# Kernel optimization log

Hardware: AMD Instinct MI355X
Metric: run time of the kernel (lower is better)

## Reference

```python
import jax, jax.numpy as jnp
import numpy as np

H = 8  # n_heads

def setup_inputs() -> dict:
    key = jax.random.key(0)
    k1, k2, k3, k4, k5 = jax.random.split(key, 5)
    B, N, D = 4, 2048, 512
    x = jax.random.normal(k1, (B, N, D), dtype=jnp.float32)
    mask_flat = jax.random.randint(k2, (B, N), 0, 2).astype(bool)
    s = 1.0 / np.sqrt(D)
    Wq = jax.random.normal(k3, (D, D), dtype=jnp.float32) * s
    Wkv = jax.random.normal(k4, (D, 2 * D), dtype=jnp.float32) * s
    Wo = jax.random.normal(k5, (D, D), dtype=jnp.float32) * s
    return {"x": x, "mask_flat": mask_flat, "Wq": Wq, "Wkv": Wkv, "Wo": Wo}

def reference(x, mask_flat, Wq, Wkv, Wo):
    B, N, D = x.shape
    d = D // H
    scale = d ** -0.5
    kv = x @ Wkv                                   # (B,N,2D)
    k, v = jnp.split(kv, 2, axis=-1)
    q = x @ Wq                                     # (B,N,D)
    # (B,H,N,d)
    q = q.reshape(B, N, H, d).transpose(0, 2, 1, 3)
    k = k.reshape(B, N, H, d).transpose(0, 2, 1, 3)
    v = v.reshape(B, N, H, d).transpose(0, 2, 1, 3)
    attn = jax.nn.softmax(jnp.einsum('bhmd,bhnd->bhmn', q, k) * scale, axis=-1)
    res = jnp.einsum('bhmn,bhnd->bhmd', attn, v)   # (B,H,N,d)
    out = res.transpose(0, 2, 1, 3).reshape(B, N, D) @ Wo
    # non-masked query positions produce zero output (residual elsewhere keeps them)
    return jnp.where(mask_flat[..., None], out, 0.0)
```

## Files before the change

kernel.cpp:

```cpp
#include <hip/hip_runtime.h>

typedef __bf16 bf16x8 __attribute__((ext_vector_type(8)));
typedef float f32x4 __attribute__((ext_vector_type(4)));
typedef float f32x16 __attribute__((ext_vector_type(16)));
typedef unsigned short u16x8 __attribute__((ext_vector_type(8)));
typedef unsigned short u16x4 __attribute__((ext_vector_type(4)));
typedef unsigned int u32x4 __attribute__((ext_vector_type(4)));
typedef int i32x2 __attribute__((ext_vector_type(2)));

__device__ inline unsigned short f2bf(float f) {
    __bf16 h = (__bf16)f;
    return __builtin_bit_cast(unsigned short, h);
}

__device__ inline unsigned int pkbf(float lo, float hi) {
    return (unsigned int)f2bf(lo) | ((unsigned int)f2bf(hi) << 16);
}

__device__ inline float fexp2(float x) {
#if __has_builtin(__builtin_amdgcn_exp2f)
    return __builtin_amdgcn_exp2f(x);
#else
    return exp2f(x);
#endif
}

__device__ inline f32x4 mfma16(u16x8 a, u16x8 b, f32x4 c) {
    return __builtin_amdgcn_mfma_f32_16x16x32_bf16(
        __builtin_bit_cast(bf16x8, a), __builtin_bit_cast(bf16x8, b), c, 0, 0, 0);
}

__device__ inline f32x16 mfma32(u16x8 a, u16x8 b, f32x16 c) {
    return __builtin_amdgcn_mfma_f32_32x32x16_bf16(
        __builtin_bit_cast(bf16x8, a), __builtin_bit_cast(bf16x8, b), c, 0, 0, 0);
}

__device__ inline i32x2 permswap(unsigned int a, unsigned int b, int hi) {
#if __has_builtin(__builtin_amdgcn_permlane32_swap)
    (void)hi;
    return __builtin_amdgcn_permlane32_swap((int)a, (int)b, false, false);
#else
    int pa_ = __shfl_xor((int)a, 32);
    int pb_ = __shfl_xor((int)b, 32);
    i32x2 r;
    r[0] = hi ? pb_ : (int)a;
    r[1] = hi ? (int)b : pa_;
    return r;
#endif
}

__device__ inline void gld_lds16(const unsigned short* gsrc, unsigned short* ldst) {
    __builtin_amdgcn_global_load_lds(
        (const __attribute__((address_space(1))) unsigned int*)gsrc,
        (__attribute__((address_space(3))) unsigned int*)ldst, 16, 0, 0);
}

#define WAIT_VM(n)                                          \
    asm volatile("s_waitcnt vmcnt(" #n ")" ::: "memory");   \
    __builtin_amdgcn_sched_barrier(0)
#define WAIT_LGKM0                                          \
    asm volatile("s_waitcnt lgkmcnt(0)" ::: "memory");      \
    __builtin_amdgcn_sched_barrier(0)
#define BARRIER                                             \
    __builtin_amdgcn_s_barrier();                           \
    __builtin_amdgcn_sched_barrier(0)

__global__ __launch_bounds__(256) void cvt_f32_bf16(const float* __restrict__ in,
                                                    unsigned short* __restrict__ out, long n) {
    long i = ((long)blockIdx.x * blockDim.x + threadIdx.x) * 4;
    if (i >= n) return;
    float4 v = *(const float4*)(in + i);
    ushort4 r;
    r.x = f2bf(v.x); r.y = f2bf(v.y); r.z = f2bf(v.z); r.w = f2bf(v.w);
    *(ushort4*)(out + i) = r;
}

__global__ __launch_bounds__(256) void prep_weights(const float* __restrict__ Wq,
                                                    const float* __restrict__ Wkv,
                                                    const float* __restrict__ Wo,
                                                    unsigned short* __restrict__ WqkvT,
                                                    unsigned short* __restrict__ WoT,
                                                    float qscale) {
    __shared__ float tile[64][65];
    const int z = blockIdx.z;
    if (z != 1 && blockIdx.x >= 8) return;
    const float* W = (z == 0) ? Wq : (z == 1) ? Wkv : Wo;
    unsigned short* Wt = (z == 0) ? WqkvT : (z == 1) ? (WqkvT + 512L * 512) : WoT;
    const int N = (z == 1) ? 1024 : 512;
    const float scale = (z == 0) ? qscale : 1.0f;
    const int K = 512;
    const int n0 = blockIdx.x * 64, k0 = blockIdx.y * 64;
    const int c = threadIdx.x & 63;
    const int r4 = threadIdx.x >> 6;
#pragma unroll
    for (int i = 0; i < 16; i++) {
        int r = r4 * 16 + i;
        tile[r][c] = W[(long)(k0 + r) * N + n0 + c];
    }
    __syncthreads();
#pragma unroll
    for (int i = 0; i < 16; i++) {
        int rr = r4 * 16 + i;
        Wt[(long)(n0 + rr) * K + k0 + c] = f2bf(tile[c][rr] * scale);
    }
}

__global__ __launch_bounds__(256) void scan_mask(const int* __restrict__ mask,
                                                 int* __restrict__ idx, int* __restrict__ cnt) {
    const int b = blockIdx.x;
    const int tid = threadIdx.x;
    __shared__ int wsum[4];
    int m[8]; int pc = 0;
#pragma unroll
    for (int k = 0; k < 8; k++) { m[k] = mask[b * 2048 + tid * 8 + k]; pc += (m[k] != 0); }
    int s = pc;
    const int lane = tid & 63;
    for (int off = 1; off < 64; off <<= 1) {
        int v = __shfl_up(s, off);
        if (lane >= off) s += v;
    }
    if (lane == 63) wsum[tid >> 6] = s;
    __syncthreads();
    int wbase = 0;
    for (int w = 0; w < (tid >> 6); w++) wbase += wsum[w];
    int run = wbase + s - pc;
#pragma unroll
    for (int k = 0; k < 8; k++) if (m[k]) idx[b * 2048 + (run++)] = tid * 8 + k;
    if (tid == 255) cnt[b] = wbase + s;
}

__global__ __launch_bounds__(256) void gemm_qkv(const unsigned short* __restrict__ A,
                                                const unsigned short* __restrict__ Bt,
                                                unsigned short* __restrict__ qkb,
                                                unsigned short* __restrict__ vT) {
    const int K = 512;
    __shared__ unsigned short AsL[2][128 * 32];
    __shared__ unsigned short BsL[2][128 * 32];
    const int tid = threadIdx.x;
    const int lane = tid & 63;
    const int wid = tid >> 6;
    const int lg = lane >> 4, lr = lane & 15;
    const int wm = wid >> 1, wn = wid & 1;
    const long m0 = (long)blockIdx.y * 128, n0 = (long)blockIdx.x * 128;

    f32x4 acc[4][4] = {};

    const unsigned short* aS0 = A  + (m0 + (tid >> 2)) * K + (tid & 3) * 8;
    const unsigned short* aS1 = A  + (m0 + 64 + (tid >> 2)) * K + (tid & 3) * 8;
    const unsigned short* bS0 = Bt + (n0 + (tid >> 2)) * K + (tid & 3) * 8;
    const unsigned short* bS1 = Bt + (n0 + 64 + (tid >> 2)) * K + (tid & 3) * 8;

#define GSTAGE(bufi, k0v)                                    \
    {                                                        \
        gld_lds16(aS0 + (k0v), &AsL[bufi][wid * 512]);       \
        gld_lds16(aS1 + (k0v), &AsL[bufi][2048 + wid * 512]);\
        gld_lds16(bS0 + (k0v), &BsL[bufi][wid * 512]);       \
        gld_lds16(bS1 + (k0v), &BsL[bufi][2048 + wid * 512]);\
    }
#define GREAD(cur)                                                                    \
    {                                                                                 \
        _Pragma("unroll")                                                             \
        for (int i = 0; i < 4; i++) {                                                 \
            af[i]  = *(const u16x8*)&AsL[cur][(wm * 64 + i * 16 + lr) * 32 + lg * 8]; \
            bfr[i] = *(const u16x8*)&BsL[cur][(wn * 64 + i * 16 + lr) * 32 + lg * 8]; \
        }                                                                             \
    }
#define GMFMA                                                                  \
    {                                                                          \
        _Pragma("unroll")                                                      \
        for (int i = 0; i < 4; i++)                                            \
            _Pragma("unroll")                                                  \
            for (int j = 0; j < 4; j++)                                        \
                acc[i][j] = mfma16(af[i], bfr[j], acc[i][j]);                  \
    }

    const int nk = K >> 5;
    GSTAGE(0, 0);
    GSTAGE(1, 32);
    for (int t = 0; t < nk - 1; t++) {
        const int cur = t & 1;
        u16x8 af[4], bfr[4];
        WAIT_VM(4);
        BARRIER;
        GREAD(cur);
        WAIT_LGKM0;
        BARRIER;
        if (t < nk - 2) GSTAGE(cur, (t + 2) * 32);
        GMFMA;
    }
    {
        u16x8 af[4], bfr[4];
        WAIT_VM(0);
        BARRIER;
        GREAD((nk - 1) & 1);
        GMFMA;
    }
#undef GSTAGE
#undef GREAD
#undef GMFMA

    if (n0 < 1024) {
#pragma unroll
        for (int i = 0; i < 4; i++)
#pragma unroll
            for (int j = 0; j < 4; j++)
#pragma unroll
                for (int r = 0; r < 4; r++) {
                    long row = m0 + wm * 64 + i * 16 + lg * 4 + r;
                    long col = n0 + wn * 64 + j * 16 + lr;
                    qkb[row * 1024 + col] = f2bf(acc[i][j][r]);
                }
    } else {
#pragma unroll
        for (int i = 0; i < 4; i++)
#pragma unroll
            for (int j = 0; j < 4; j++) {
                long vd = n0 - 1024 + wn * 64 + j * 16 + lr;
                long tok0 = m0 + wm * 64 + i * 16 + lg * 4;
                u16x4 st;
#pragma unroll
                for (int r = 0; r < 4; r++) st[r] = f2bf(acc[i][j][r]);
                *(u16x4*)&vT[vd * 8192 + tok0] = st;
            }
    }
}

template<int WRITE_BF16, int MASKED>
__global__ __launch_bounds__(256) void gemm_bt(const unsigned short* __restrict__ A,
                                               const unsigned short* __restrict__ Bt,
                                               void* __restrict__ Cv,
                                               int M, int N, int K,
                                               const int* __restrict__ mask) {
    __shared__ unsigned short AsL[2][128 * 32];
    __shared__ unsigned short BsL[2][128 * 32];
    const int tid = threadIdx.x;
    const int lane = tid & 63;
    const int wid = tid >> 6;
    const int lg = lane >> 4, lr = lane & 15;
    const int wm = wid >> 1, wn = wid & 1;
    const long m0 = (long)blockIdx.y * 128, n0 = (long)blockIdx.x * 128;

    f32x4 acc[4][4] = {};

    const unsigned short* aS0 = A  + (m0 + (tid >> 2)) * K + (tid & 3) * 8;
    const unsigned short* aS1 = A  + (m0 + 64 + (tid >> 2)) * K + (tid & 3) * 8;
    const unsigned short* bS0 = Bt + (n0 + (tid >> 2)) * K + (tid & 3) * 8;
    const unsigned short* bS1 = Bt + (n0 + 64 + (tid >> 2)) * K + (tid & 3) * 8;

#define GSTAGE(bufi, k0v)                                    \
    {                                                        \
        gld_lds16(aS0 + (k0v), &AsL[bufi][wid * 512]);       \
        gld_lds16(aS1 + (k0v), &AsL[bufi][2048 + wid * 512]);\
        gld_lds16(bS0 + (k0v), &BsL[bufi][wid * 512]);       \
        gld_lds16(bS1 + (k0v), &BsL[bufi][2048 + wid * 512]);\
    }
#define GREAD(cur)                                                                    \
    {                                                                                 \
        _Pragma("unroll")                                                             \
        for (int i = 0; i < 4; i++) {                                                 \
            af[i]  = *(const u16x8*)&AsL[cur][(wm * 64 + i * 16 + lr) * 32 + lg * 8]; \
            bfr[i] = *(const u16x8*)&BsL[cur][(wn * 64 + i * 16 + lr) * 32 + lg * 8]; \
        }                                                                             \
    }
#define GMFMA                                                                  \
    {                                                                          \
        _Pragma("unroll")                                                      \
        for (int i = 0; i < 4; i++)                                            \
            _Pragma("unroll")                                                  \
            for (int j = 0; j < 4; j++)                                        \
                acc[i][j] = mfma16(af[i], bfr[j], acc[i][j]);                  \
    }

    const int nk = K >> 5;
    GSTAGE(0, 0);
    GSTAGE(1, 32);
    for (int t = 0; t < nk - 1; t++) {
        const int cur = t & 1;
        u16x8 af[4], bfr[4];
        WAIT_VM(4);
        BARRIER;
        GREAD(cur);
        WAIT_LGKM0;
        BARRIER;
        if (t < nk - 2) GSTAGE(cur, (t + 2) * 32);
        GMFMA;
    }
    {
        u16x8 af[4], bfr[4];
        WAIT_VM(0);
        BARRIER;
        GREAD((nk - 1) & 1);
        GMFMA;
    }
#undef GSTAGE
#undef GREAD
#undef GMFMA

#pragma unroll
    for (int i = 0; i < 4; i++)
#pragma unroll
        for (int j = 0; j < 4; j++)
#pragma unroll
            for (int r = 0; r < 4; r++) {
                long row = m0 + wm * 64 + i * 16 + lg * 4 + r;
                long col = n0 + wn * 64 + j * 16 + lr;
                float v = acc[i][j][r];
                if (MASKED) {
                    if (!mask[row]) v = 0.0f;
                    ((float*)Cv)[row * N + col] = v;
                } else if (WRITE_BF16) {
                    ((unsigned short*)Cv)[row * N + col] = f2bf(v);
                } else {
                    ((float*)Cv)[row * N + col] = v;
                }
            }
}

__global__ __launch_bounds__(256) void attn_kernel(const unsigned short* __restrict__ qk,
                                                   const unsigned short* __restrict__ vT,
                                                   unsigned short* __restrict__ res,
                                                   const int* __restrict__ idxm,
                                                   const int* __restrict__ cntm) {
    const int Nseq = 2048, LD = 1024;
    const long T = 8192;
    const int id = blockIdx.x;
    const int xcd = id & 7, jj = id >> 3;
    const int g = xcd + 8 * (jj & 3);
    const int qt = jj >> 2;
    const int b = g >> 3, h = g & 7;

    const int count = cntm[b];
    if (qt * 64 >= count) return;

    const int tid = threadIdx.x;
    const int wid = tid >> 6, lane = tid & 63;
    const int qL = lane & 31, hi = lane >> 5;
    const int qh = wid >> 1, kvh = wid & 1;

    __shared__ unsigned short LDSB[2][2][8192];

    const int i_q = qt * 64 + qh * 32 + qL;
    const int gi = idxm[b * 2048 + (i_q < count ? i_q : count - 1)];
    const long qrow = (long)b * Nseq + gi;
    u16x8 qf[4];
#pragma unroll
    for (int j = 0; j < 4; j++)
        qf[j] = *(const u16x8*)(qk + qrow * LD + h * 64 + 16 * j + 8 * hi);

    f32x16 oacc[2] = {};
    f32x16 lacc = {};
    u16x8 onesf;
#pragma unroll
    for (int e = 0; e < 8; e++) onesf[e] = 0x3F80;

    const int Rs = lane >> 3, p0 = lane & 7;
    const int psw = (p0 ^ Rs) * 8;
    const unsigned short* kS = qk + 512 + ((long)b * Nseq + kvh * 1024 + 32 * qh + Rs) * LD
                               + h * 64 + psw;
    const unsigned short* vS = vT + ((long)h * 64 + 32 * qh + Rs) * T + (long)b * Nseq
                               + kvh * 1024 + psw;
    const int rsw = qL & 7;

#define STAGE(bufi)                                                             \
    {                                                                           \
        _Pragma("unroll")                                                       \
        for (int i = 0; i < 4; i++)                                             \
            gld_lds16(kS + (long)i * 8 * LD,                                    \
                      &LDSB[kvh][bufi][(qh * 4 + i) * 512]);                    \
        _Pragma("unroll")                                                       \
        for (int i = 0; i < 4; i++)                                             \
            gld_lds16(vS + (long)i * 8 * T,                                     \
                      &LDSB[kvh][bufi][4096 + (qh * 4 + i) * 512]);             \
        kS += 64L * LD; vS += 64;                                               \
    }

#define READ_KF(buf)                                                            \
    {                                                                           \
        _Pragma("unroll")                                                       \
        for (int kvb = 0; kvb < 2; kvb++)                                       \
            _Pragma("unroll")                                                   \
            for (int j = 0; j < 4; j++)                                         \
                kf[kvb][j] = *(const u16x8*)&LDSB[kvh][buf][(kvb * 32 + qL) * 64\
                                             + (((2 * j + hi) ^ rsw) * 8)];     \
    }
#define READ_VF(buf)                                                            \
    {                                                                           \
        _Pragma("unroll")                                                       \
        for (int db = 0; db < 2; db++)                                          \
            _Pragma("unroll")                                                   \
            for (int jk = 0; jk < 4; jk++)                                      \
                vf[db][jk] = *(const u16x8*)&LDSB[kvh][buf][4096                \
                                 + (db * 32 + qL) * 64                          \
                                 + (((2 * jk + hi) ^ rsw) * 8)];                \
    }

#define QKNEXT(SN)                                                              \
    {                                                                           \
        SN[0] = (f32x16){}; SN[1] = (f32x16){};                                 \
        _Pragma("unroll")                                                       \
        for (int j = 0; j < 4; j++) {                                           \
            SN[0] = mfma32(kf[0][j], qf[j], SN[0]);                             \
            SN[1] = mfma32(kf[1][j], qf[j], SN[1]);                             \
        }                                                                       \
    }

#define PACK_PV(SC)                                                                    \
    {                                                                                  \
        u16x8 pa[4];                                                                   \
        _Pragma("unroll")                                                              \
        for (int kvb = 0; kvb < 2; kvb++) {                                            \
            unsigned int w[8];                                                         \
            _Pragma("unroll")                                                          \
            for (int i = 0; i < 8; i++)                                                \
                w[i] = pkbf(fexp2(SC[kvb][2 * i]), fexp2(SC[kvb][2 * i + 1]));         \
            _Pragma("unroll")                                                          \
            for (int hh = 0; hh < 2; hh++) {                                           \
                i32x2 ra = permswap(w[4 * hh + 0], w[4 * hh + 2], hi);                 \
                i32x2 rb = permswap(w[4 * hh + 1], w[4 * hh + 3], hi);                 \
                u32x4 fw;                                                              \
                fw[0] = (unsigned)ra[0]; fw[1] = (unsigned)rb[0];                      \
                fw[2] = (unsigned)ra[1]; fw[3] = (unsigned)rb[1];                      \
                pa[kvb * 2 + hh] = __builtin_bit_cast(u16x8, fw);                      \
            }                                                                          \
        }                                                                              \
        _Pragma("unroll")                                                              \
        for (int jk = 0; jk < 4; jk++) {                                               \
            lacc = mfma32(pa[jk], onesf, lacc);                                        \
            oacc[0] = mfma32(pa[jk], vf[0][jk], oacc[0]);                              \
            oacc[1] = mfma32(pa[jk], vf[1][jk], oacc[1]);                              \
        }                                                                              \
    }

#define STEP(SC, SN, cur)                                                       \
    {                                                                           \
        WAIT_VM(4);          \
        BARRIER;                                             \
        READ_KF(cur ^ 1);                                                       \
        READ_VF(cur);                                                           \
        WAIT_LGKM0;                                                             \
        BARRIER;                \
        STAGE(cur);                                                             \
        QKNEXT(SN);                                                             \
        PACK_PV(SC);                                                            \
    }

    u16x8 kf[2][4], vf[2][4];
    f32x16 sA[2], sB[2];

    STAGE(0);
    STAGE(1);
    WAIT_VM(12);
    BARRIER;
    READ_KF(0);
    WAIT_LGKM0;
    QKNEXT(sA);

    for (int t = 0; t < 14; t += 2) {
        STEP(sA, sB, 0);
        STEP(sB, sA, 1);
    }
    {
        WAIT_VM(4);
        BARRIER;
        READ_KF(1);
        READ_VF(0);
        WAIT_LGKM0;
        QKNEXT(sB);
        PACK_PV(sA);
    }
    {
        WAIT_VM(0);
        BARRIER;
        READ_VF(1);
        WAIT_LGKM0;
        PACK_PV(sB);
    }
#undef STAGE
#undef READ_KF
#undef READ_VF
#undef QKNEXT
#undef PACK_PV
#undef STEP

    __syncthreads();
    float* Ox = (float*)&LDSB[0][0][0];
    float* lX = Ox + 2 * 32 * 65;

    if (kvh == 1) {
#pragma unroll
        for (int reg = 0; reg < 16; reg++) {
            const int crow = (reg & 3) + 8 * (reg >> 2) + 4 * hi;
            Ox[qh * 2080 + crow * 65 + qL]      = oacc[0][reg];
            Ox[qh * 2080 + crow * 65 + 32 + qL] = oacc[1][reg];
            lX[qh * 32 + crow] = lacc[reg];
        }
    }
    __syncthreads();
    if (kvh == 0) {
#pragma unroll
        for (int reg = 0; reg < 16; reg++) {
            const int crow = (reg & 3) + 8 * (reg >> 2) + 4 * hi;
            const int row_c = qt * 64 + qh * 32 + crow;
            if (row_c < count) {
                float lt = lacc[reg] + lX[qh * 32 + crow];
                float linv = 1.0f / lt;
                float o0 = oacc[0][reg] + Ox[qh * 2080 + crow * 65 + qL];
                float o1 = oacc[1][reg] + Ox[qh * 2080 + crow * 65 + 32 + qL];
                const int orig = idxm[b * 2048 + row_c];
                long row = (long)b * Nseq + orig;
                res[row * 512 + h * 64 + qL]      = f2bf(o0 * linv);
                res[row * 512 + h * 64 + 32 + qL] = f2bf(o1 * linv);
            }
        }
    }
}

extern "C" void kernel_launch(void* const* d_in, const int* in_sizes, int n_in,
                              void* d_out, int out_size, void* d_ws, size_t ws_size,
                              hipStream_t stream) {
    const float* x   = (const float*)d_in[0];
    const int* mask  = (const int*)d_in[1];
    const float* Wq  = (const float*)d_in[2];
    const float* Wkv = (const float*)d_in[3];
    const float* Wo  = (const float*)d_in[4];
    float* out = (float*)d_out;

    const int Nseq = 2048, D = 512;
    const long T = 8192;
    const float QSCALE = 0.125f * 1.4426950408889634f;

    unsigned short* ws    = (unsigned short*)d_ws;
    unsigned short* xb    = ws;
    unsigned short* WqkvT = xb    + T * D;
    unsigned short* WoT   = WqkvT + 1536L * 512;
    unsigned short* qkb   = WoT   + 512L * 512;
    unsigned short* vTb   = qkb   + T * 1024;
    unsigned short* resb  = vTb   + 512L * T;
    int* idxb = (int*)(resb + T * 512);
    int* cntb = idxb + 4 * 2048;

    cvt_f32_bf16<<<(int)(T * D / 1024), 256, 0, stream>>>(x, xb, T * D);
    prep_weights<<<dim3(16, 8, 3), 256, 0, stream>>>(Wq, Wkv, Wo, WqkvT, WoT, QSCALE);
    scan_mask<<<4, 256, 0, stream>>>(mask, idxb, cntb);

    gemm_qkv<<<dim3(12, 64), 256, 0, stream>>>(xb, WqkvT, qkb, vTb);

    attn_kernel<<<1024, 256, 0, stream>>>(qkb, vTb, resb, idxb, cntb);

    gemm_bt<0, 1><<<dim3(4, 64), 256, 0, stream>>>(resb, WoT, out, T, D, D, mask);
}
```

Measured before the change: 94.07 us.

## Merge preprocessing kernels into one launch and narrow output GEMM tile

The three preprocessing kernels (x conversion to bf16, weight transpose/convert, mask scan) are merged into one launch that dispatches on block index, cutting two kernel launches and their gaps. The output projection GEMM is specialised to a 128x64 tile, which doubles its grid from 256 to 512 blocks so more CUs are busy. The narrower tile reuses the A operand less and adds a shared-memory allocation to the merged kernel for the branches that don't need it.

```diff
diff --git a/kernel.cpp b/kernel.cpp
--- a/kernel.cpp
+++ b/kernel.cpp
@@ -65,68 +65,71 @@
     __builtin_amdgcn_s_barrier();                           \
     __builtin_amdgcn_sched_barrier(0)
 
-__global__ __launch_bounds__(256) void cvt_f32_bf16(const float* __restrict__ in,
-                                                    unsigned short* __restrict__ out, long n) {
-    long i = ((long)blockIdx.x * blockDim.x + threadIdx.x) * 4;
-    if (i >= n) return;
-    float4 v = *(const float4*)(in + i);
-    ushort4 r;
-    r.x = f2bf(v.x); r.y = f2bf(v.y); r.z = f2bf(v.z); r.w = f2bf(v.w);
-    *(ushort4*)(out + i) = r;
-}
-
-__global__ __launch_bounds__(256) void prep_weights(const float* __restrict__ Wq,
-                                                    const float* __restrict__ Wkv,
-                                                    const float* __restrict__ Wo,
-                                                    unsigned short* __restrict__ WqkvT,
-                                                    unsigned short* __restrict__ WoT,
-                                                    float qscale) {
+__global__ __launch_bounds__(256) void preamble(const float* __restrict__ x,
+                                                unsigned short* __restrict__ xb,
+                                                const float* __restrict__ Wq,
+                                                const float* __restrict__ Wkv,
+                                                const float* __restrict__ Wo,
+                                                unsigned short* __restrict__ WqkvT,
+                                                unsigned short* __restrict__ WoT,
+                                                float qscale,
+                                                const int* __restrict__ mask,
+                                                int* __restrict__ idx,
+                                                int* __restrict__ cnt) {
     __shared__ float tile[64][65];
-    const int z = blockIdx.z;
-    if (z != 1 && blockIdx.x >= 8) return;
-    const float* W = (z == 0) ? Wq : (z == 1) ? Wkv : Wo;
-    unsigned short* Wt = (z == 0) ? WqkvT : (z == 1) ? (WqkvT + 512L * 512) : WoT;
-    const int N = (z == 1) ? 1024 : 512;
-    const float scale = (z == 0) ? qscale : 1.0f;
-    const int K = 512;
-    const int n0 = blockIdx.x * 64, k0 = blockIdx.y * 64;
-    const int c = threadIdx.x & 63;
-    const int r4 = threadIdx.x >> 6;
-#pragma unroll
-    for (int i = 0; i < 16; i++) {
-        int r = r4 * 16 + i;
-        tile[r][c] = W[(long)(k0 + r) * N + n0 + c];
-    }
-    __syncthreads();
-#pragma unroll
-    for (int i = 0; i < 16; i++) {
-        int rr = r4 * 16 + i;
-        Wt[(long)(n0 + rr) * K + k0 + c] = f2bf(tile[c][rr] * scale);
-    }
-}
-
-__global__ __launch_bounds__(256) void scan_mask(const int* __restrict__ mask,
-                                                 int* __restrict__ idx, int* __restrict__ cnt) {
-    const int b = blockIdx.x;
+    __shared__ int wsum[4];
+    const int bid = blockIdx.x;
     const int tid = threadIdx.x;
-    __shared__ int wsum[4];
-    int m[8]; int pc = 0;
-#pragma unroll
-    for (int k = 0; k < 8; k++) { m[k] = mask[b * 2048 + tid * 8 + k]; pc += (m[k] != 0); }
-    int s = pc;
-    const int lane = tid & 63;
-    for (int off = 1; off < 64; off <<= 1) {
-        int v = __shfl_up(s, off);
-        if (lane >= off) s += v;
-    }
-    if (lane == 63) wsum[tid >> 6] = s;
-    __syncthreads();
-    int wbase = 0;
-    for (int w = 0; w < (tid >> 6); w++) wbase += wsum[w];
-    int run = wbase + s - pc;
-#pragma unroll
-    for (int k = 0; k < 8; k++) if (m[k]) idx[b * 2048 + (run++)] = tid * 8 + k;
-    if (tid == 255) cnt[b] = wbase + s;
+
+    if (bid < 4096) {
+        long i = ((long)bid * 256 + tid) * 4;
+        float4 v = *(const float4*)(x + i);
+        ushort4 r;
+        r.x = f2bf(v.x); r.y = f2bf(v.y); r.z = f2bf(v.z); r.w = f2bf(v.w);
+        *(ushort4*)(xb + i) = r;
+    } else if (bid < 4480) {
+        const int flat = bid - 4096;
+        const int z = flat >> 7;
+        const int by = (flat >> 4) & 7, bx = flat & 15;
+        if (z != 1 && bx >= 8) return;
+        const float* W = (z == 0) ? Wq : (z == 1) ? Wkv : Wo;
+        unsigned short* Wt = (z == 0) ? WqkvT : (z == 1) ? (WqkvT + 512L * 512) : WoT;
+        const int N = (z == 1) ? 1024 : 512;
+        const float scale = (z == 0) ? qscale : 1.0f;
+        const int n0 = bx * 64, k0 = by * 64;
+        const int c = tid & 63;
+        const int r4 = tid >> 6;
+#pragma unroll
+        for (int i = 0; i < 16; i++) {
+            int r = r4 * 16 + i;
+            tile[r][c] = W[(long)(k0 + r) * N + n0 + c];
+        }
+        __syncthreads();
+#pragma unroll
+        for (int i = 0; i < 16; i++) {
+            int rr = r4 * 16 + i;
+            Wt[(long)(n0 + rr) * 512 + k0 + c] = f2bf(tile[c][rr] * scale);
+        }
+    } else {
+        const int b = bid - 4480;
+        int m[8]; int pc = 0;
+#pragma unroll
+        for (int k = 0; k < 8; k++) { m[k] = mask[b * 2048 + tid * 8 + k]; pc += (m[k] != 0); }
+        int s = pc;
+        const int lane = tid & 63;
+        for (int off = 1; off < 64; off <<= 1) {
+            int v = __shfl_up(s, off);
+            if (lane >= off) s += v;
+        }
+        if (lane == 63) wsum[tid >> 6] = s;
+        __syncthreads();
+        int wbase = 0;
+        for (int w = 0; w < (tid >> 6); w++) wbase += wsum[w];
+        int run = wbase + s - pc;
+#pragma unroll
+        for (int k = 0; k < 8; k++) if (m[k]) idx[b * 2048 + (run++)] = tid * 8 + k;
+        if (tid == 255) cnt[b] = wbase + s;
+    }
 }
 
 __global__ __launch_bounds__(256) void gemm_qkv(const unsigned short* __restrict__ A,
@@ -225,49 +228,47 @@
     }
 }
 
-template<int WRITE_BF16, int MASKED>
-__global__ __launch_bounds__(256) void gemm_bt(const unsigned short* __restrict__ A,
-                                               const unsigned short* __restrict__ Bt,
-                                               void* __restrict__ Cv,
-                                               int M, int N, int K,
-                                               const int* __restrict__ mask) {
+__global__ __launch_bounds__(256) void gemm_out(const unsigned short* __restrict__ A,
+                                                const unsigned short* __restrict__ Bt,
+                                                float* __restrict__ Cv,
+                                                const int* __restrict__ mask) {
+    const int K = 512, N = 512;
     __shared__ unsigned short AsL[2][128 * 32];
-    __shared__ unsigned short BsL[2][128 * 32];
+    __shared__ unsigned short BsL[2][64 * 32];
     const int tid = threadIdx.x;
     const int lane = tid & 63;
     const int wid = tid >> 6;
     const int lg = lane >> 4, lr = lane & 15;
     const int wm = wid >> 1, wn = wid & 1;
-    const long m0 = (long)blockIdx.y * 128, n0 = (long)blockIdx.x * 128;
-
-    f32x4 acc[4][4] = {};
+    const long m0 = (long)blockIdx.y * 128, n0 = (long)blockIdx.x * 64;
+
+    f32x4 acc[4][2] = {};
 
     const unsigned short* aS0 = A  + (m0 + (tid >> 2)) * K + (tid & 3) * 8;
     const unsigned short* aS1 = A  + (m0 + 64 + (tid >> 2)) * K + (tid & 3) * 8;
     const unsigned short* bS0 = Bt + (n0 + (tid >> 2)) * K + (tid & 3) * 8;
-    const unsigned short* bS1 = Bt + (n0 + 64 + (tid >> 2)) * K + (tid & 3) * 8;
 
 #define GSTAGE(bufi, k0v)                                    \
     {                                                        \
         gld_lds16(aS0 + (k0v), &AsL[bufi][wid * 512]);       \
         gld_lds16(aS1 + (k0v), &AsL[bufi][2048 + wid * 512]);\
         gld_lds16(bS0 + (k0v), &BsL[bufi][wid * 512]);       \
-        gld_lds16(bS1 + (k0v), &BsL[bufi][2048 + wid * 512]);\
     }
 #define GREAD(cur)                                                                    \
     {                                                                                 \
         _Pragma("unroll")                                                             \
-        for (int i = 0; i < 4; i++) {                                                 \
+        for (int i = 0; i < 4; i++)                                                   \
             af[i]  = *(const u16x8*)&AsL[cur][(wm * 64 + i * 16 + lr) * 32 + lg * 8]; \
-            bfr[i] = *(const u16x8*)&BsL[cur][(wn * 64 + i * 16 + lr) * 32 + lg * 8]; \
-        }                                                                             \
+        _Pragma("unroll")                                                             \
+        for (int j = 0; j < 2; j++)                                                   \
+            bfr[j] = *(const u16x8*)&BsL[cur][(wn * 32 + j * 16 + lr) * 32 + lg * 8]; \
     }
 #define GMFMA                                                                  \
     {                                                                          \
         _Pragma("unroll")                                                      \
         for (int i = 0; i < 4; i++)                                            \
             _Pragma("unroll")                                                  \
-            for (int j = 0; j < 4; j++)                                        \
+            for (int j = 0; j < 2; j++)                                        \
                 acc[i][j] = mfma16(af[i], bfr[j], acc[i][j]);                  \
     }
 
@@ -276,8 +277,8 @@
     GSTAGE(1, 32);
     for (int t = 0; t < nk - 1; t++) {
         const int cur = t & 1;
-        u16x8 af[4], bfr[4];
-        WAIT_VM(4);
+        u16x8 af[4], bfr[2];
+        WAIT_VM(3);
         BARRIER;
         GREAD(cur);
         WAIT_LGKM0;
@@ -286,7 +287,7 @@
         GMFMA;
     }
     {
-        u16x8 af[4], bfr[4];
+        u16x8 af[4], bfr[2];
         WAIT_VM(0);
         BARRIER;
         GREAD((nk - 1) & 1);
@@ -299,20 +300,14 @@
 #pragma unroll
     for (int i = 0; i < 4; i++)
 #pragma unroll
-        for (int j = 0; j < 4; j++)
+        for (int j = 0; j < 2; j++)
 #pragma unroll
             for (int r = 0; r < 4; r++) {
                 long row = m0 + wm * 64 + i * 16 + lg * 4 + r;
-                long col = n0 + wn * 64 + j * 16 + lr;
+                long col = n0 + wn * 32 + j * 16 + lr;
                 float v = acc[i][j][r];
-                if (MASKED) {
-                    if (!mask[row]) v = 0.0f;
-                    ((float*)Cv)[row * N + col] = v;
-                } else if (WRITE_BF16) {
-                    ((unsigned short*)Cv)[row * N + col] = f2bf(v);
-                } else {
-                    ((float*)Cv)[row * N + col] = v;
-                }
+                if (!mask[row]) v = 0.0f;
+                Cv[row * N + col] = v;
             }
 }
 
@@ -525,7 +520,7 @@
     const float* Wo  = (const float*)d_in[4];
     float* out = (float*)d_out;
 
-    const int Nseq = 2048, D = 512;
+    const int D = 512;
     const long T = 8192;
     const float QSCALE = 0.125f * 1.4426950408889634f;
 
@@ -539,13 +534,12 @@
     int* idxb = (int*)(resb + T * 512);
     int* cntb = idxb + 4 * 2048;
 
-    cvt_f32_bf16<<<(int)(T * D / 1024), 256, 0, stream>>>(x, xb, T * D);
-    prep_weights<<<dim3(16, 8, 3), 256, 0, stream>>>(Wq, Wkv, Wo, WqkvT, WoT, QSCALE);
-    scan_mask<<<4, 256, 0, stream>>>(mask, idxb, cntb);
+    preamble<<<4484, 256, 0, stream>>>(x, xb, Wq, Wkv, Wo, WqkvT, WoT, QSCALE,
+                                       mask, idxb, cntb);
 
     gemm_qkv<<<dim3(12, 64), 256, 0, stream>>>(xb, WqkvT, qkb, vTb);
 
     attn_kernel<<<1024, 256, 0, stream>>>(qkb, vTb, resb, idxb, cntb);
 
-    gemm_bt<0, 1><<<dim3(4, 64), 256, 0, stream>>>(resb, WoT, out, T, D, D, mask);
-}
+    gemm_out<<<dim3(8, 64), 256, 0, stream>>>(resb, WoT, out, mask);
+}
```

Measured after the change: 91.04 us. 3.2% less time.
